# Kernel tuning notes

Hardware: AMD Instinct MI355X
Metric: run time of the kernel (lower is better)

## Reference

```python
import jax, jax.numpy as jnp
import numpy as np
from jax.scipy.special import erf, digamma, i0

B, L, D, H = 4, 4096, 512, 4
_MAX_SQRT_GRADIENT = 1000.0

@jax.custom_vjp
def sqrt_bound(x):
    return jnp.sqrt(x)

def _sb_fwd(x):
    return jnp.sqrt(x), x

def _sb_bwd(x, g):
    return (g / jnp.sqrt(jnp.clip(4.0 * x, 1.0 / _MAX_SQRT_GRADIENT**2, None)),)

sqrt_bound.defvjp(_sb_fwd, _sb_bwd)

def block_diag_linear(x, w):
    # x: [..., D], w: [h, bw, bw] block-diagonal weight
    h, bw, _ = w.shape
    xr = x.reshape(x.shape[:-1] + (h, bw))
    return jnp.einsum('...hi,hij->...hj', xr, w).reshape(x.shape)

def self_att_pool(x, num_heads):
    n_state = x.shape[-1] // num_heads
    attn = jax.nn.softmax(jnp.einsum('bld,bmd->blm', x, x) / np.float32(np.sqrt(n_state)), axis=-1)
    # max over the sequence axis of the attended values, keepdims -> [B,1,D]
    return jnp.max(jnp.einsum('blm,bmd->bld', attn, x), axis=-2, keepdims=True)

def ripple_transform_hybrid(t, mix_params):
    mix = jax.nn.softmax(mix_params)
    return mix[0] * digamma(t + 1.0) + mix[1] * i0(t)

def ripple_act(data, alpha, beta, mix_params, temperature=1.0):
    def f(d):
        norm = erf(d / (jnp.max(d) * alpha))
        return jnp.sum(ripple_transform_hybrid(norm * beta, mix_params))
    g = jnp.clip(jax.grad(f)(data), -1.0, 1.0)
    return jax.nn.softmax(-g / temperature, axis=-1)  # softmin

def ripplemoe_act(data, weights, alphas, beta, mix_params, temperature=1.0):
    def f(d):
        dmax = jnp.max(d)
        norm = erf(d[None] / (dmax * alphas[:, None, None]))  # [S,B,L]
        t = ripple_transform_hybrid(norm * beta, mix_params)
        w = jax.nn.softmax(weights)
        return jnp.sum(w[:, None, None] * t)
    g = jnp.clip(jax.grad(f)(data), -1.0, 1.0)
    return jax.nn.softmax(-g / temperature, axis=-1)  # softmin

def token_selection(x, cls_w, cls_b, token_weights, prelu_a, ts_weights, ts_alphas, ts_beta, ts_mix):
    scores = jnp.einsum('bld,sd->sbl', x, cls_w) + cls_b[:, None, None]  # [S,B,L]
    p = jnp.where(scores >= 0, scores, prelu_a * scores)  # PReLU
    ts = jax.nn.celu(p) * jax.nn.silu(p) + jax.nn.gelu(p, approximate=False)
    combined = jnp.einsum('s,sbl->bl', jax.nn.selu(token_weights[:, 0]), ts)
    _, idx = jax.lax.top_k(combined, combined.shape[-1])  # k = L, descending permutation
    vals = ts.sum(0)  # [B,L]
    b_idx = jnp.arange(combined.shape[0])[:, None]
    importance = jnp.ones_like(combined).at[b_idx, idx].add(vals)
    return (1.0 + ripplemoe_act(importance, ts_weights, ts_alphas, ts_beta, ts_mix))[..., None]

def _forward(x, attention_space, W_spatial, W_sil, W_ohead, W_out, w_ig, w_ag, a_param,
             cls_w, cls_b, token_weights, prelu_a, ts_weights, ts_alphas, ts_beta, ts_mix,
             pa1_alpha, pa1_beta, pa1_mix, pa2_alpha, pa2_beta, pa2_mix):
    spatial = jnp.einsum('bld,de->ble', x, attention_space) @ W_spatial.T
    # RG-LRU style gating
    gate_x = jax.nn.sigmoid(block_diag_linear(x, w_ig))
    gate_a = jax.nn.sigmoid(block_diag_linear(x, w_ag))
    log_a = -8.0 * jax.nn.softplus(a_param) * gate_a
    normalized_x = x * gate_x * sqrt_bound(1.0 - jnp.exp(2.0 * log_a))
    gated = jnp.exp(log_a) * self_att_pool(spatial, H) + normalized_x
    sparsity = ripple_act(gated @ W_sil.T, pa1_alpha, pa1_beta, pa1_mix)
    attn = (gated * sparsity) @ W_ohead.T
    sel = token_selection(x, cls_w, cls_b, token_weights, prelu_a, ts_weights, ts_alphas, ts_beta, ts_mix)
    out = ripple_act(attn * sel, pa2_alpha, pa2_beta, pa2_mix)
    return out @ W_out.T

def setup_inputs() -> dict:
    key = jax.random.key(0)
    ks = jax.random.split(key, 12)
    lim = float(1.0 / np.sqrt(D))
    xav = float(np.sqrt(6.0 / (2 * D)))
    bw = D // H
    u = jax.random.uniform(ks[8], (D,), jnp.float32, 0.9**2 + 1e-8, 0.999**2 + 1e-8)
    return {
        'x': jax.random.normal(ks[0], (B, L, D), jnp.float32),
        'attention_space': jax.random.uniform(ks[1], (D, D), jnp.float32, -xav, xav),
        'W_spatial': jax.random.uniform(ks[2], (D, D), jnp.float32, -lim, lim),
        'W_sil': jax.random.uniform(ks[3], (D, D), jnp.float32, -lim, lim),
        'W_ohead': jax.random.uniform(ks[4], (D, D), jnp.float32, -lim, lim),
        'W_out': jax.random.uniform(ks[5], (D, D), jnp.float32, -lim, lim),
        'w_ig': jax.random.normal(ks[6], (H, bw, bw), jnp.float32) * np.float32(np.sqrt(1.0 / bw)),
        'w_ag': jax.random.normal(ks[7], (H, bw, bw), jnp.float32) * np.float32(np.sqrt(1.0 / bw)),
        'a_param': jnp.log(jnp.exp(-0.5 * jnp.log(u)) - 1.0),
        'cls_w': jax.random.uniform(ks[9], (H, D), jnp.float32, -lim, lim),
        'cls_b': jax.random.uniform(ks[10], (H,), jnp.float32, -lim, lim),
        'token_weights': jax.random.normal(ks[11], (H, 1), jnp.float32),
        'prelu_a': jnp.array(0.25, jnp.float32),
        'ts_weights': jnp.ones(H, jnp.float32) / H,
        'ts_alphas': jnp.ones(H, jnp.float32),
        'ts_beta': jnp.array(1.0, jnp.float32),
        'ts_mix': jnp.full((2,), 0.5, jnp.float32),
        'pa1_alpha': jnp.array(1.0, jnp.float32),
        'pa1_beta': jnp.array(1.0, jnp.float32),
        'pa1_mix': jnp.full((2,), 0.5, jnp.float32),
        'pa2_alpha': jnp.array(1.0, jnp.float32),
        'pa2_beta': jnp.array(1.0, jnp.float32),
        'pa2_mix': jnp.full((2,), 0.5, jnp.float32),
    }

def reference(x, attention_space, W_spatial, W_sil, W_ohead, W_out, w_ig, w_ag, a_param,
              cls_w, cls_b, token_weights, prelu_a, ts_weights, ts_alphas, ts_beta, ts_mix,
              pa1_alpha, pa1_beta, pa1_mix, pa2_alpha, pa2_beta, pa2_mix):
    return _forward(x, attention_space, W_spatial, W_sil, W_ohead, W_out, w_ig, w_ag, a_param,
                    cls_w, cls_b, token_weights, prelu_a, ts_weights, ts_alphas, ts_beta, ts_mix,
                    pa1_alpha, pa1_beta, pa1_mix, pa2_alpha, pa2_beta, pa2_mix)
```

## Files before the change

### kernel.cpp

```cpp
#include <hip/hip_runtime.h>

typedef unsigned short ushort;
typedef unsigned int uint;
typedef unsigned long long u64;

#define DEV __device__ __forceinline__

typedef __attribute__((ext_vector_type(4))) float f32x4;
typedef __bf16 bf16x8 __attribute__((ext_vector_type(8)));
typedef __attribute__((ext_vector_type(4))) ushort u16x4;
typedef __attribute__((ext_vector_type(8))) ushort u16x8;

static constexpr int B_ = 4, L_ = 4096, D_ = 512;
static constexpr long NE = (long)B_ * L_ * D_;

DEV float b2f(ushort u) { return __uint_as_float(((uint)u) << 16); }
DEV ushort f2b(float f) {
    uint u = __float_as_uint(f);
    uint r = u + 0x7FFFu + ((u >> 16) & 1u);
    return (ushort)(r >> 16);
}
DEV uint mapF(float f) {
    uint b = __float_as_uint(f);
    return (b & 0x80000000u) ? ~b : (b | 0x80000000u);
}
DEV float unmapF(uint u) {
    uint b = (u & 0x80000000u) ? (u & 0x7FFFFFFFu) : ~u;
    return __uint_as_float(b);
}
DEV float rcp_(float x) { return __builtin_amdgcn_rcpf(x); }
DEV float fexp(float x) { return __builtin_amdgcn_exp2f(x * 1.44269504089f); }
DEV float sigm(float x) { return rcp_(1.f + fexp(-x)); }

DEV void gload16(const ushort* g, ushort* l) {
    __builtin_amdgcn_global_load_lds((const __attribute__((address_space(1))) void*)g,
                                     (__attribute__((address_space(3))) void*)l, 16, 0, 0);
}

DEV float trigamma1p(float t) {
    float x = t + 1.f;
    float acc = 0.f;
#pragma unroll
    for (int k = 0; k < 6; k++) { float xx = x + (float)k; acc += rcp_(xx * xx); }
    float y = x + 6.f;
    float iy = rcp_(y), iy2 = iy * iy;
    return acc + iy * (1.f + iy * (0.5f + iy * (0.166666667f + iy2 * (-0.0333333333f + iy2 * 0.0238095238f))));
}
DEV float besselI1(float t) {
    float q = 0.25f * t * t;
    return 0.5f * t * (1.f + q * (0.5f + q * (0.0833333333f + q * (0.00694444444f + q * (3.47222222e-4f + q * 1.15740741e-5f)))));
}
DEV float rippleH(float u, float beta, float mix0, float mix1) {
    float t = beta * erff(u);
    float Tp = mix0 * trigamma1p(t) + mix1 * besselI1(t);
    float ep = 1.12837917f * fexp(-u * u);
    return beta * Tp * ep;
}

DEV void gemm_core(const ushort* __restrict__ A, int lda,
                   const ushort* __restrict__ Bt, int ldb, int K,
                   ushort* __restrict__ Alds, ushort* __restrict__ Blds,
                   f32x4 (&acc)[4][4])
{
    const int tid = threadIdx.x;
    const int lane = tid & 63;
    const int wave = tid >> 6;
    const int wr = wave >> 1, wc = wave & 1;

    const int srow = wave * 16 + (lane >> 2);
    const int skc = (lane & 3) * 8;
    const ushort* Ag0 = A + (size_t)srow * lda + skc;
    const ushort* Ag1 = A + (size_t)(srow + 64) * lda + skc;
    const ushort* Bg0 = Bt + (size_t)srow * ldb + skc;
    const ushort* Bg1 = Bt + (size_t)(srow + 64) * ldb + skc;
    ushort* Al0 = Alds + wave * 512;
    ushort* Al1 = Alds + 2048 + wave * 512;
    ushort* Bl0 = Blds + wave * 512;
    ushort* Bl1 = Blds + 2048 + wave * 512;

    const int ar = wr * 64 + (lane & 15);
    const int br = wc * 64 + (lane & 15);
    const int kk = (lane >> 4) * 8;

    for (int k0 = 0; k0 < K; k0 += 32) {
        __syncthreads();
        gload16(Ag0 + k0, Al0);
        gload16(Ag1 + k0, Al1);
        gload16(Bg0 + k0, Bl0);
        gload16(Bg1 + k0, Bl1);
        __syncthreads();
        bf16x8 af[4], bfr[4];
#pragma unroll
        for (int mi = 0; mi < 4; mi++) af[mi] = *(const bf16x8*)&Alds[(ar + mi * 16) * 32 + kk];
#pragma unroll
        for (int ni = 0; ni < 4; ni++) bfr[ni] = *(const bf16x8*)&Blds[(br + ni * 16) * 32 + kk];
#pragma unroll
        for (int mi = 0; mi < 4; mi++)
#pragma unroll
            for (int ni = 0; ni < 4; ni++)
                acc[mi][ni] = __builtin_amdgcn_mfma_f32_16x16x32_bf16(af[mi], bfr[ni], acc[mi][ni], 0, 0, 0);
    }
}

template <int MODE, bool DOMAX>
__global__ __launch_bounds__(256, 2) void gemm_bt(
    const ushort* __restrict__ A, int lda,
    const ushort* __restrict__ Bt, int ldb,
    void* __restrict__ Cv, int ldc, int K,
    const float* __restrict__ rowScale, u64* __restrict__ pmax)
{
    __shared__ ushort Alds[128 * 32];
    __shared__ ushort Blds[128 * 32];
    const int row0 = blockIdx.y * 128, col0 = blockIdx.x * 128;
    f32x4 acc[4][4] = {};
    gemm_core(A + (size_t)row0 * lda, lda, Bt + (size_t)col0 * ldb, ldb, K, Alds, Blds, acc);

    const int tid = threadIdx.x;
    const int lane = tid & 63;
    const int wave = tid >> 6;
    const int wr = wave >> 1, wc = wave & 1;
    const int ocol = col0 + wc * 64 + (lane & 15);
    u64 lp = 0;
#pragma unroll
    for (int mi = 0; mi < 4; mi++) {
        const int rbase = row0 + wr * 64 + mi * 16 + (lane >> 4) * 4;
#pragma unroll
        for (int j = 0; j < 4; j++) {
            float sc = (MODE == 3) ? rowScale[rbase + j] : 1.f;
#pragma unroll
            for (int ni = 0; ni < 4; ni++) {
                float v = acc[mi][ni][j] * sc;
                int cc = ocol + ni * 16;
                if (MODE == 1) ((ushort*)Cv)[(size_t)(rbase + j) * ldc + cc] = f2b(v);
                else ((float*)Cv)[(size_t)(rbase + j) * ldc + cc] = v;
                if (DOMAX) {
                    uint idx = (uint)((rbase + j) * ldc + cc);
                    u64 p = ((u64)mapF(v) << 32) | (u64)(~idx);
                    lp = (p > lp) ? p : lp;
                }
            }
        }
    }
    if (DOMAX) {
#pragma unroll
        for (int off = 32; off > 0; off >>= 1) {
            u64 o = __shfl_xor(lp, off);
            lp = (o > lp) ? o : lp;
        }
        if (lane == 0) atomicMax(pmax, lp);
    }
}

__global__ __launch_bounds__(256, 2) void pv_split_k(const ushort* __restrict__ P, const ushort* __restrict__ Vt,
                                                     float* __restrict__ part)
{
    __shared__ ushort Alds[128 * 32];
    __shared__ ushort Blds[128 * 32];
    const int ks = blockIdx.z;
    const int row0 = blockIdx.y * 128, col0 = blockIdx.x * 128;
    f32x4 acc[4][4] = {};
    gemm_core(P + (size_t)row0 * 4096 + ks * 1024, 4096,
              Vt + (size_t)col0 * 4096 + ks * 1024, 4096, 1024, Alds, Blds, acc);

    float* C = part + (size_t)ks * 2097152 + (size_t)row0 * 512 + col0;
    const int tid = threadIdx.x;
    const int lane = tid & 63;
    const int wave = tid >> 6;
    const int wr = wave >> 1, wc = wave & 1;
    const int ocol = wc * 64 + (lane & 15);
#pragma unroll
    for (int mi = 0; mi < 4; mi++) {
        const int rl = wr * 64 + mi * 16 + (lane >> 4) * 4;
#pragma unroll
        for (int j = 0; j < 4; j++)
#pragma unroll
            for (int ni = 0; ni < 4; ni++)
                C[(size_t)(rl + j) * 512 + ocol + ni * 16] = acc[mi][ni][j];
    }
}

__global__ __launch_bounds__(256) void pool_combine_k(const float* __restrict__ part, uint* __restrict__ poolU)
{
    const int tid = threadIdx.x;
    const int l0 = blockIdx.x * 32;
    float m0 = -3.4e38f, m1 = -3.4e38f;
    for (int l = 0; l < 32; l++) {
        size_t off = (size_t)(l0 + l) * 512;
        float s0 = 0.f, s1 = 0.f;
#pragma unroll
        for (int ks = 0; ks < 4; ks++) {
            s0 += part[(size_t)ks * 2097152 + off + tid];
            s1 += part[(size_t)ks * 2097152 + off + tid + 256];
        }
        m0 = fmaxf(m0, s0); m1 = fmaxf(m1, s1);
    }
    atomicMax(&poolU[tid], mapF(m0));
    atomicMax(&poolU[tid + 256], mapF(m1));
}

__global__ __launch_bounds__(256, 2) void gate_gemm_k(const ushort* __restrict__ xb,
                                                      const ushort* __restrict__ wigT, const ushort* __restrict__ wagT,
                                                      ushort* __restrict__ gxab, ushort* __restrict__ gaab)
{
    __shared__ ushort Alds[128 * 32];
    __shared__ ushort Blds[128 * 32];
    const int which = blockIdx.x;
    const int h = blockIdx.z;
    const ushort* A = xb + (size_t)blockIdx.y * 128 * 512 + h * 128;
    const ushort* W = (which ? wagT : wigT) + (size_t)h * 16384;
    f32x4 acc[4][4] = {};
    gemm_core(A, 512, W, 128, 128, Alds, Blds, acc);

    ushort* C = (which ? gaab : gxab) + (size_t)blockIdx.y * 128 * 512 + h * 128;
    const int tid = threadIdx.x;
    const int lane = tid & 63;
    const int wave = tid >> 6;
    const int wr = wave >> 1, wc = wave & 1;
    const int ocol = wc * 64 + (lane & 15);
#pragma unroll
    for (int mi = 0; mi < 4; mi++) {
        const int rl = wr * 64 + mi * 16 + (lane >> 4) * 4;
#pragma unroll
        for (int j = 0; j < 4; j++)
#pragma unroll
            for (int ni = 0; ni < 4; ni++)
                C[(size_t)(rl + j) * 512 + ocol + ni * 16] = f2b(acc[mi][ni][j]);
    }
}

__global__ void convert_f2b_k(const float* __restrict__ s, ushort* __restrict__ d, long n4) {
    long i = (long)blockIdx.x * blockDim.x + threadIdx.x;
    long st = (long)gridDim.x * blockDim.x;
    for (; i < n4; i += st) {
        f32x4 v = ((const f32x4*)s)[i];
        u16x4 o;
        o[0] = f2b(v[0]); o[1] = f2b(v[1]); o[2] = f2b(v[2]); o[3] = f2b(v[3]);
        ((u16x4*)d)[i] = o;
    }
}

__global__ void convert_w4_k(const float* __restrict__ w0, const float* __restrict__ w1,
                             const float* __restrict__ w2, const float* __restrict__ w3,
                             ushort* __restrict__ dst) {
    const float* srcs[4] = {w0, w1, w2, w3};
    const float* s = srcs[blockIdx.y];
    ushort* d = dst + (size_t)blockIdx.y * 262144;
    int i = blockIdx.x * 256 + threadIdx.x;
    f32x4 v = ((const f32x4*)s)[i];
    u16x4 o;
    o[0] = f2b(v[0]); o[1] = f2b(v[1]); o[2] = f2b(v[2]); o[3] = f2b(v[3]);
    ((u16x4*)d)[i] = o;
}

template <bool SRCF32>
__global__ __launch_bounds__(256) void transpose_to_bf16(const void* __restrict__ srcv, ushort* __restrict__ dst, int R, int C) {
    __shared__ float tile[32][33];
    const int z = blockIdx.z;
    const float* sf = (const float*)srcv + (size_t)z * R * C;
    const ushort* sb = (const ushort*)srcv + (size_t)z * R * C;
    ushort* dz = dst + (size_t)z * R * C;
    const int tx = threadIdx.x & 31, ty = threadIdx.x >> 5;
    const int c = blockIdx.x * 32 + tx;
#pragma unroll
    for (int k = 0; k < 4; k++) {
        const int r = blockIdx.y * 32 + ty + k * 8;
        tile[ty + k * 8][tx] = SRCF32 ? sf[(size_t)r * C + c] : b2f(sb[(size_t)r * C + c]);
    }
    __syncthreads();
#pragma unroll
    for (int k = 0; k < 4; k++) {
        const int dr = blockIdx.x * 32 + ty + k * 8;
        const int dc = blockIdx.y * 32 + tx;
        dz[(size_t)dr * R + dc] = f2b(tile[tx][ty + k * 8]);
    }
}

__global__ __launch_bounds__(256) void transpose_gates_k(const float* __restrict__ wig, const float* __restrict__ wag,
                                                         ushort* __restrict__ wigT, ushort* __restrict__ wagT) {
    __shared__ float tile[32][33];
    const int which = blockIdx.z >> 2, h = blockIdx.z & 3;
    const float* src = (which ? wag : wig) + (size_t)h * 16384;
    ushort* dst = (which ? wagT : wigT) + (size_t)h * 16384;
    const int tx = threadIdx.x & 31, ty = threadIdx.x >> 5;
    const int c = blockIdx.x * 32 + tx;
#pragma unroll
    for (int k = 0; k < 4; k++) {
        const int r = blockIdx.y * 32 + ty + k * 8;
        tile[ty + k * 8][tx] = src[(size_t)r * 128 + c];
    }
    __syncthreads();
#pragma unroll
    for (int k = 0; k < 4; k++) {
        const int dr = blockIdx.x * 32 + ty + k * 8;
        const int dc = blockIdx.y * 32 + tx;
        dst[(size_t)dr * 128 + dc] = f2b(tile[tx][ty + k * 8]);
    }
}

__global__ void init_misc_k(uint* poolU, u64* pmax) {
    int i = blockIdx.x * 256 + threadIdx.x;
    if (i < 2048) poolU[i] = 0u;
    if (i < 4) pmax[i] = 0ull;
}
__global__ void sentinel_k(float* o) { o[threadIdx.x] = 1.0e6f; }

__global__ __launch_bounds__(256) void gates_gated_k(const float* __restrict__ x, const ushort* __restrict__ gxab,
                                                     const ushort* __restrict__ gaab, const float* __restrict__ a_param,
                                                     const uint* __restrict__ poolU, ushort* __restrict__ gatedb) {
    __shared__ float sp8[512];
    const int tid = threadIdx.x;
    for (int d = tid; d < 512; d += 256) {
        float a = a_param[d];
        sp8[d] = 8.f * (fmaxf(a, 0.f) + log1pf(expf(-fabsf(a))));
    }
    __syncthreads();
    long i = (long)blockIdx.x * blockDim.x + tid;
    long st = (long)gridDim.x * blockDim.x;
    const long n8 = NE >> 3;
    for (; i < n8; i += st) {
        u16x8 gx8 = ((const u16x8*)gxab)[i];
        u16x8 ga8 = ((const u16x8*)gaab)[i];
        f32x4 x0 = ((const f32x4*)x)[2 * i];
        f32x4 x1 = ((const f32x4*)x)[2 * i + 1];
        long e = i << 3;
        int b = (int)(e >> 21);
        int d0 = (int)(e & 511);
        u16x8 o;
#pragma unroll
        for (int j = 0; j < 8; j++) {
            float xv = (j < 4) ? x0[j] : x1[j - 4];
            float gx = sigm(b2f(gx8[j]));
            float ga = sigm(b2f(ga8[j]));
            float la = -sp8[d0 + j] * ga;
            float ea = fexp(la);
            float nx = xv * gx * sqrtf(fmaxf(1.f - fexp(2.f * la), 0.f));
            float pl = unmapF(poolU[b * 512 + d0 + j]);
            o[j] = f2b(ea * pl + nx);
        }
        ((u16x8*)gatedb)[i] = o;
    }
}

__global__ __launch_bounds__(256) void softmax_rows_k(const ushort* __restrict__ S, ushort* __restrict__ P, float scale) {
    __shared__ float red[256];
    const int tid = threadIdx.x;
    const ushort* row = S + (size_t)blockIdx.x * 4096;
    float vals[16];
    bf16x8 v0 = *(const bf16x8*)&row[tid * 16];
    bf16x8 v1 = *(const bf16x8*)&row[tid * 16 + 8];
    float mx = -3.4e38f;
#pragma unroll
    for (int k = 0; k < 8; k++) { vals[k] = (float)v0[k] * scale; mx = fmaxf(mx, vals[k]); }
#pragma unroll
    for (int k = 0; k < 8; k++) { vals[8 + k] = (float)v1[k] * scale; mx = fmaxf(mx, vals[8 + k]); }
    red[tid] = mx; __syncthreads();
    for (int s = 128; s > 0; s >>= 1) { if (tid < s) red[tid] = fmaxf(red[tid], red[tid + s]); __syncthreads(); }
    mx = red[0]; __syncthreads();
    float sum = 0.f;
#pragma unroll
    for (int k = 0; k < 16; k++) { vals[k] = fexp(vals[k] - mx); sum += vals[k]; }
    red[tid] = sum; __syncthreads();
    for (int s = 128; s > 0; s >>= 1) { if (tid < s) red[tid] += red[tid + s]; __syncthreads(); }
    float inv = rcp_(red[0]);
    ushort* prow = P + (size_t)blockIdx.x * 4096;
#pragma unroll
    for (int k = 0; k < 16; k++) prow[tid * 16 + k] = f2b(vals[k] * inv);
}

__global__ __launch_bounds__(256) void redmax1_k(const float* __restrict__ d, long n, float* __restrict__ bmax, int* __restrict__ bidx) {
    __shared__ float rv[256];
    __shared__ int ri[256];
    const int tid = threadIdx.x;
    long g = (long)blockIdx.x * 256 + tid;
    const long stride = (long)gridDim.x * 256;
    float bv = -3.4e38f; int bi = -1;
    for (long i = g; i < n; i += stride) {
        float v = d[i];
        if (v > bv) { bv = v; bi = (int)i; }
    }
    rv[tid] = bv; ri[tid] = bi; __syncthreads();
    for (int s = 128; s > 0; s >>= 1) {
        if (tid < s) {
            float ov = rv[tid + s]; int oi = ri[tid + s];
            if (oi >= 0 && (ri[tid] < 0 || ov > rv[tid] || (ov == rv[tid] && oi < ri[tid]))) { rv[tid] = ov; ri[tid] = oi; }
        }
        __syncthreads();
    }
    if (tid == 0) { bmax[blockIdx.x] = rv[0]; bidx[blockIdx.x] = ri[0]; }
}
__global__ __launch_bounds__(256) void redmax2_k(const float* __restrict__ bmax, const int* __restrict__ bidx, int n,
                                                 float* __restrict__ outM, int* __restrict__ outI) {
    __shared__ float rv[256];
    __shared__ int ri[256];
    const int tid = threadIdx.x;
    float bv = -3.4e38f; int bi = -1;
    for (int i = tid; i < n; i += 256) {
        float v = bmax[i]; int ix = bidx[i];
        if (ix >= 0 && (bi < 0 || v > bv || (v == bv && ix < bi))) { bv = v; bi = ix; }
    }
    rv[tid] = bv; ri[tid] = bi; __syncthreads();
    for (int s = 128; s > 0; s >>= 1) {
        if (tid < s) {
            float ov = rv[tid + s]; int oi = ri[tid + s];
            if (oi >= 0 && (ri[tid] < 0 || ov > rv[tid] || (ov == rv[tid] && oi < ri[tid]))) { rv[tid] = ov; ri[tid] = oi; }
        }
        __syncthreads();
    }
    if (tid == 0) { outM[0] = rv[0]; outI[0] = ri[0]; }
}

__global__ __launch_bounds__(256) void ripple_g_k(const float* __restrict__ d, float* __restrict__ gb, float* __restrict__ sspart,
                                                  const u64* __restrict__ pmax, const float* __restrict__ alpha_p,
                                                  const float* __restrict__ beta_p, const float* __restrict__ mix_p) {
    __shared__ float red[256];
    const int tid = threadIdx.x;
    const float M = unmapF((uint)(pmax[0] >> 32));
    const float alpha = alpha_p[0], beta = beta_p[0];
    float m0 = mix_p[0], m1 = mix_p[1];
    float mm = fmaxf(m0, m1);
    float e0 = fexp(m0 - mm), e1 = fexp(m1 - mm);
    float inv = rcp_(e0 + e1);
    float mix0 = e0 * inv, mix1 = e1 * inv;
    const float invMA = rcp_(M * alpha);
    float ss = 0.f;
    long g = (long)blockIdx.x * 256 + tid;
    const long stride = (long)gridDim.x * 256;
    for (long i = g; i < NE; i += stride) {
        float dv = d[i];
        float H = rippleH(dv * invMA, beta, mix0, mix1);
        gb[i] = H * invMA;
        ss += H * dv;
    }
    red[tid] = ss; __syncthreads();
    for (int s = 128; s > 0; s >>= 1) { if (tid < s) red[tid] += red[tid + s]; __syncthreads(); }
    if (tid == 0) sspart[blockIdx.x] = red[0];
}
__global__ __launch_bounds__(256) void redsum2_k(const float* __restrict__ part, int n, float* __restrict__ out) {
    __shared__ float red[256];
    const int tid = threadIdx.x;
    float s = 0.f;
    for (int i = tid; i < n; i += 256) s += part[i];
    red[tid] = s; __syncthreads();
    for (int q = 128; q > 0; q >>= 1) { if (tid < q) red[tid] += red[tid + q]; __syncthreads(); }
    if (tid == 0) out[0] = red[0];
}

template <int GS>
__global__ __launch_bounds__(256) void ripple_softmax_k(const float* __restrict__ gb,
                                                        const u64* __restrict__ pmax,
                                                        const float* __restrict__ ssTot, const float* __restrict__ alpha_p,
                                                        const ushort* __restrict__ gatedb, ushort* __restrict__ outb) {
    __shared__ float red[256];
    const int tid = threadIdx.x;
    const float M = unmapF((uint)(pmax[0] >> 32));
    const int amax = (int)(~(uint)(pmax[0] & 0xFFFFFFFFull));
    const float corr = ssTot[0] * rcp_(M * M * alpha_p[0]);
    long base = (long)blockIdx.x * 512;
    float g0 = gb[base + tid];
    float g1 = gb[base + tid + 256];
    if ((int)(base + tid) == amax) g0 -= corr;
    if ((int)(base + tid + 256) == amax) g1 -= corr;
    g0 = fminf(fmaxf(g0, -1.f), 1.f);
    g1 = fminf(fmaxf(g1, -1.f), 1.f);
    float mn = fminf(g0, g1);
    red[tid] = mn; __syncthreads();
    for (int s = 128; s > 0; s >>= 1) { if (tid < s) red[tid] = fminf(red[tid], red[tid + s]); __syncthreads(); }
    mn = red[0]; __syncthreads();
    float e0 = fexp(mn - g0), e1 = fexp(mn - g1);
    red[tid] = e0 + e1; __syncthreads();
    for (int s = 128; s > 0; s >>= 1) { if (tid < s) red[tid] += red[tid + s]; __syncthreads(); }
    float inv = rcp_(red[0]);
    if (GS) {
        outb[base + tid] = f2b(b2f(gatedb[base + tid]) * (e0 * inv));
        outb[base + tid + 256] = f2b(b2f(gatedb[base + tid + 256]) * (e1 * inv));
    } else {
        outb[base + tid] = f2b(e0 * inv);
        outb[base + tid + 256] = f2b(e1 * inv);
    }
}

__global__ __launch_bounds__(256) void ts1_k(const float* __restrict__ x, const float* __restrict__ cls_w,
                                             const float* __restrict__ cls_b, const float* __restrict__ tw,
                                             const float* __restrict__ prelu_a,
                                             float* __restrict__ combined, float* __restrict__ vals) {
    __shared__ float cw[2048];
    const int tid = threadIdx.x;
    for (int i = tid; i < 2048; i += 256) cw[i] = cls_w[i];
    __syncthreads();
    const int lane = tid & 63, wid = tid >> 6;
    const int row = blockIdx.x * 4 + wid;
    const float* xr = x + (size_t)row * 512 + lane * 8;
    float pa0 = 0, pa1 = 0, pa2 = 0, pa3 = 0;
#pragma unroll
    for (int j = 0; j < 8; j++) {
        float v = xr[j];
        int c = lane * 8 + j;
        pa0 += v * cw[c]; pa1 += v * cw[512 + c]; pa2 += v * cw[1024 + c]; pa3 += v * cw[1536 + c];
    }
#pragma unroll
    for (int o = 32; o > 0; o >>= 1) {
        pa0 += __shfl_down(pa0, o); pa1 += __shfl_down(pa1, o);
        pa2 += __shfl_down(pa2, o); pa3 += __shfl_down(pa3, o);
    }
    if (lane == 0) {
        float a = prelu_a[0];
        float sc[4] = {pa0, pa1, pa2, pa3};
        float comb = 0.f, vsum = 0.f;
#pragma unroll
        for (int s = 0; s < 4; s++) {
            float p = sc[s] + cls_b[s];
            p = (p >= 0.f) ? p : a * p;
            float cel = (p > 0.f) ? p : expm1f(p);
            float sil = p * sigm(p);
            float gel = 0.5f * p * (1.f + erff(p * 0.70710678f));
            float ts = cel * sil + gel;
            float ww = tw[s];
            float se = 1.05070099f * ((ww > 0.f) ? ww : 1.67326324f * expm1f(ww));
            comb += se * ts;
            vsum += ts;
        }
        combined[row] = comb;
        vals[row] = vsum;
    }
}

__global__ __launch_bounds__(256) void ts2a_k(const float* __restrict__ combined, int* __restrict__ rankp) {
    __shared__ float q[512];
    const int b = blockIdx.z;
    const int tid = threadIdx.x;
    const float* cr = combined + b * 4096;
    const int q0 = blockIdx.y * 512;
    for (int i = tid; i < 512; i += 256) q[i] = cr[q0 + i];
    __syncthreads();
    const int p = blockIdx.x * 256 + tid;
    const float cp = cr[p];
    const f32x4* q4 = (const f32x4*)q;
    int rank = 0;
#pragma unroll 8
    for (int i4 = 0; i4 < 128; i4++) {
        f32x4 v = q4[i4];
        int qb = q0 + i4 * 4;
        rank += (v[0] > cp) || (v[0] == cp && (qb + 0) < p);
        rank += (v[1] > cp) || (v[1] == cp && (qb + 1) < p);
        rank += (v[2] > cp) || (v[2] == cp && (qb + 2) < p);
        rank += (v[3] > cp) || (v[3] == cp && (qb + 3) < p);
    }
    rankp[((b * 8 + blockIdx.y) * 4096) + p] = rank;
}

__global__ __launch_bounds__(256) void ts2b_k(const int* __restrict__ rankp, const float* __restrict__ vals,
                                              float* __restrict__ imp) {
    const int b = blockIdx.y;
    const int p = blockIdx.x * 256 + threadIdx.x;
    int rank = 0;
#pragma unroll
    for (int c = 0; c < 8; c++) rank += rankp[((b * 8 + c) * 4096) + p];
    imp[b * 4096 + p] = 1.f + vals[b * 4096 + rank];
}

__global__ __launch_bounds__(256) void moe_g_k(const float* __restrict__ imp, float* __restrict__ gmoe,
                                               float* __restrict__ sspart, const float* __restrict__ scalM,
                                               const float* __restrict__ tsw, const float* __restrict__ tsa,
                                               const float* __restrict__ tsb, const float* __restrict__ tsmix) {
    __shared__ float red[256];
    const int tid = threadIdx.x;
    const float M = scalM[0];
    float w[4], invMA[4], invA[4];
    {
        float wm = fmaxf(fmaxf(tsw[0], tsw[1]), fmaxf(tsw[2], tsw[3]));
        float s = 0.f;
#pragma unroll
        for (int k = 0; k < 4; k++) { w[k] = fexp(tsw[k] - wm); s += w[k]; }
        float si = rcp_(s);
#pragma unroll
        for (int k = 0; k < 4; k++) { w[k] *= si; invMA[k] = rcp_(M * tsa[k]); invA[k] = rcp_(tsa[k]); }
    }
    const float beta = tsb[0];
    float m0 = tsmix[0], m1 = tsmix[1];
    float mm = fmaxf(m0, m1);
    float e0 = fexp(m0 - mm), e1 = fexp(m1 - mm);
    float minv = rcp_(e0 + e1);
    const float mix0 = e0 * minv, mix1 = e1 * minv;

    float ss = 0.f;
    int i = blockIdx.x * 256 + tid;
    const int stride = gridDim.x * 256;
    for (; i < 65536; i += stride) {
        float dv = imp[i];
        float gbv = 0.f;
#pragma unroll
        for (int s = 0; s < 4; s++) {
            float H = rippleH(dv * invMA[s], beta, mix0, mix1);
            gbv += w[s] * H * invMA[s];
            ss += w[s] * H * dv * invA[s];
        }
        gmoe[i] = gbv;
    }
    red[tid] = ss; __syncthreads();
    for (int s = 128; s > 0; s >>= 1) { if (tid < s) red[tid] += red[tid + s]; __syncthreads(); }
    if (tid == 0) sspart[blockIdx.x] = red[0];
}

__global__ __launch_bounds__(256) void moe_sel_k(const float* __restrict__ gmoe, const float* __restrict__ scalM,
                                                 const int* __restrict__ scalI, const float* __restrict__ ssTot,
                                                 float* __restrict__ sel) {
    __shared__ float red[256];
    const int tid = threadIdx.x;
    const int b = blockIdx.x;
    const float M = scalM[0];
    const int amax = scalI[0];
    const float corr = ssTot[0] * rcp_(M * M);
    float g[16];
    float mn = 3.4e38f;
#pragma unroll
    for (int k = 0; k < 16; k++) {
        int i = b * 4096 + tid + k * 256;
        float v = gmoe[i];
        if (i == amax) v -= corr;
        v = fminf(fmaxf(v, -1.f), 1.f);
        g[k] = v;
        mn = fminf(mn, v);
    }
    red[tid] = mn; __syncthreads();
    for (int s = 128; s > 0; s >>= 1) { if (tid < s) red[tid] = fminf(red[tid], red[tid + s]); __syncthreads(); }
    mn = red[0]; __syncthreads();
    float sum = 0.f;
#pragma unroll
    for (int k = 0; k < 16; k++) { g[k] = fexp(mn - g[k]); sum += g[k]; }
    red[tid] = sum; __syncthreads();
    for (int s = 128; s > 0; s >>= 1) { if (tid < s) red[tid] += red[tid + s]; __syncthreads(); }
    float inv = rcp_(red[0]);
#pragma unroll
    for (int k = 0; k < 16; k++) sel[b * 4096 + tid + k * 256] = 1.f + g[k] * inv;
}

static constexpr size_t OFF_XB    = 0;
static constexpr size_t OFF_TMPB  = 16777216;
static constexpr size_t OFF_SPB   = 33554432;
static constexpr size_t OFF_SPT   = 50331648;
static constexpr size_t OFF_DBUF  = 67108864;
static constexpr size_t OFF_HBUF  = 100663296;
static constexpr size_t OFF_GATB  = 134217728;
static constexpr size_t OFF_NXB   = 150994944;
static constexpr size_t OFF_EAB   = 167772160;
static constexpr size_t OFF_AST   = 184549376;
static constexpr size_t OFF_WSP   = 185073664;
static constexpr size_t OFF_WSIL  = 185597952;
static constexpr size_t OFF_WOH   = 186122240;
static constexpr size_t OFF_WOUT  = 186646528;
static constexpr size_t OFF_WIGT  = 187170816;
static constexpr size_t OFF_WAGT  = 187301888;
static constexpr size_t OFF_POOL  = 187432960;
static constexpr size_t OFF_SCAL  = 187441152;
static constexpr size_t OFF_SCALI = 187441408;
static constexpr size_t OFF_BMAX  = 187441664;
static constexpr size_t OFF_BIDX  = 187449856;
static constexpr size_t OFF_SSP   = 187458048;
static constexpr size_t OFF_COMB  = 187466240;
static constexpr size_t OFF_VALS  = 187728384;
static constexpr size_t OFF_IMP   = 187990528;
static constexpr size_t OFF_GMOE  = 188252672;
static constexpr size_t OFF_SEL   = 188514816;
static constexpr size_t WS_NEED   = 188776960;

extern "C" void kernel_launch(void* const* d_in, const int* in_sizes, int n_in,
                              void* d_out, int out_size, void* d_ws, size_t ws_size,
                              hipStream_t stream)
{
    (void)in_sizes; (void)n_in; (void)out_size;
    const float* x    = (const float*)d_in[0];
    const float* AS   = (const float*)d_in[1];
    const float* Wsp  = (const float*)d_in[2];
    const float* Wsil = (const float*)d_in[3];
    const float* Woh  = (const float*)d_in[4];
    const float* Wout = (const float*)d_in[5];
    const float* wig  = (const float*)d_in[6];
    const float* wag  = (const float*)d_in[7];
    const float* a_param = (const float*)d_in[8];
    const float* cls_w = (const float*)d_in[9];
    const float* cls_b = (const float*)d_in[10];
    const float* tokw  = (const float*)d_in[11];
    const float* prelu = (const float*)d_in[12];
    const float* tsw   = (const float*)d_in[13];
    const float* tsa   = (const float*)d_in[14];
    const float* tsb   = (const float*)d_in[15];
    const float* tsmix = (const float*)d_in[16];
    const float* p1a = (const float*)d_in[17];
    const float* p1b = (const float*)d_in[18];
    const float* p1m = (const float*)d_in[19];
    const float* p2a = (const float*)d_in[20];
    const float* p2b = (const float*)d_in[21];
    const float* p2m = (const float*)d_in[22];
    float* out = (float*)d_out;

    char* w = (char*)d_ws;
    if (ws_size < WS_NEED) { sentinel_k<<<1, 256, 0, stream>>>(out); return; }

    ushort* xb    = (ushort*)(w + OFF_XB);
    ushort* tmpb  = (ushort*)(w + OFF_TMPB);
    ushort* spb   = (ushort*)(w + OFF_SPB);
    ushort* spT   = (ushort*)(w + OFF_SPT);
    float*  dbuf  = (float*)(w + OFF_DBUF);
    float*  Hbuf  = (float*)(w + OFF_HBUF);
    ushort* Sb    = (ushort*)(w + OFF_DBUF);
    ushort* Pb    = (ushort*)(w + OFF_HBUF);
    float*  pvpart= (float*)(w + OFF_XB);
    int*    rankp = (int*)(w + OFF_DBUF);
    ushort* gatedb= (ushort*)(w + OFF_GATB);
    ushort* gxab  = (ushort*)(w + OFF_NXB);
    ushort* gaab  = (ushort*)(w + OFF_EAB);
    ushort* ASt   = (ushort*)(w + OFF_AST);
    ushort* Wspb  = (ushort*)(w + OFF_WSP);
    ushort* Wsilb = (ushort*)(w + OFF_WSIL);
    ushort* Wohb  = (ushort*)(w + OFF_WOH);
    ushort* Woutb = (ushort*)(w + OFF_WOUT);
    ushort* wigT  = (ushort*)(w + OFF_WIGT);
    ushort* wagT  = (ushort*)(w + OFF_WAGT);
    uint*   poolU = (uint*)(w + OFF_POOL);
    float*  scal  = (float*)(w + OFF_SCAL);
    u64*    pmax  = (u64*)(w + OFF_SCAL + 128);
    int*    scalI = (int*)(w + OFF_SCALI);
    float*  bmax  = (float*)(w + OFF_BMAX);
    int*    bidx  = (int*)(w + OFF_BIDX);
    float*  sspart= (float*)(w + OFF_SSP);
    float*  comb  = (float*)(w + OFF_COMB);
    float*  vals  = (float*)(w + OFF_VALS);
    float*  imp   = (float*)(w + OFF_IMP);
    float*  gmoe  = (float*)(w + OFF_GMOE);
    float*  sel   = (float*)(w + OFF_SEL);
    ushort* gsb     = tmpb;
    ushort* probs2b = xb;

    convert_f2b_k<<<2048, 256, 0, stream>>>(x, xb, NE >> 2);
    convert_w4_k<<<dim3(256, 4), 256, 0, stream>>>(Wsp, Wsil, Woh, Wout, Wspb);
    transpose_to_bf16<true><<<dim3(16, 16, 1), 256, 0, stream>>>(AS, ASt, 512, 512);
    transpose_gates_k<<<dim3(4, 4, 8), 256, 0, stream>>>(wig, wag, wigT, wagT);
    init_misc_k<<<8, 256, 0, stream>>>(poolU, pmax);

    gate_gemm_k<<<dim3(2, 128, 4), 256, 0, stream>>>(xb, wigT, wagT, gxab, gaab);

    gemm_bt<1, false><<<dim3(4, 128), 256, 0, stream>>>(xb, 512, ASt, 512, tmpb, 512, 512, nullptr, nullptr);
    gemm_bt<1, false><<<dim3(4, 128), 256, 0, stream>>>(tmpb, 512, Wspb, 512, spb, 512, 512, nullptr, nullptr);

    transpose_to_bf16<false><<<dim3(16, 128, 4), 256, 0, stream>>>(spb, spT, 4096, 512);
    const float sc128 = 0.0883883476f;
    for (int b = 0; b < 4; b++) {
        const ushort* spB = spb + (size_t)b * L_ * D_;
        gemm_bt<1, false><<<dim3(32, 32), 256, 0, stream>>>(spB, 512, spB, 512, Sb, 4096, 512, nullptr, nullptr);
        softmax_rows_k<<<4096, 256, 0, stream>>>(Sb, Pb, sc128);
        pv_split_k<<<dim3(4, 32, 4), 256, 0, stream>>>(Pb, spT + (size_t)b * D_ * L_, pvpart);
        pool_combine_k<<<128, 256, 0, stream>>>(pvpart, poolU + b * 512);
    }

    gates_gated_k<<<1024, 256, 0, stream>>>(x, gxab, gaab, a_param, poolU, gatedb);

    gemm_bt<0, true><<<dim3(4, 128), 256, 0, stream>>>(gatedb, 512, Wsilb, 512, dbuf, 512, 512, nullptr, &pmax[0]);
    ripple_g_k<<<2048, 256, 0, stream>>>(dbuf, Hbuf, sspart, &pmax[0], p1a, p1b, p1m);
    redsum2_k<<<1, 256, 0, stream>>>(sspart, 2048, &scal[1]);
    ripple_softmax_k<1><<<16384, 256, 0, stream>>>(Hbuf, &pmax[0], &scal[1], p1a, gatedb, gsb);

    ts1_k<<<4096, 256, 0, stream>>>(x, cls_w, cls_b, tokw, prelu, comb, vals);
    ts2a_k<<<dim3(16, 8, 4), 256, 0, stream>>>(comb, rankp);
    ts2b_k<<<dim3(16, 4), 256, 0, stream>>>(rankp, vals, imp);
    redmax1_k<<<64, 256, 0, stream>>>(imp, 65536, bmax, bidx);
    redmax2_k<<<1, 256, 0, stream>>>(bmax, bidx, 64, &scal[4], &scalI[2]);
    moe_g_k<<<64, 256, 0, stream>>>(imp, gmoe, sspart, &scal[4], tsw, tsa, tsb, tsmix);
    redsum2_k<<<1, 256, 0, stream>>>(sspart, 64, &scal[5]);
    moe_sel_k<<<4, 256, 0, stream>>>(gmoe, &scal[4], &scalI[2], &scal[5], sel);

    gemm_bt<3, true><<<dim3(4, 128), 256, 0, stream>>>(gsb, 512, Wohb, 512, dbuf, 512, 512, sel, &pmax[1]);

    ripple_g_k<<<2048, 256, 0, stream>>>(dbuf, Hbuf, sspart, &pmax[1], p2a, p2b, p2m);
    redsum2_k<<<1, 256, 0, stream>>>(sspart, 2048, &scal[3]);
    ripple_softmax_k<0><<<16384, 256, 0, stream>>>(Hbuf, &pmax[1], &scal[3], p2a, nullptr, probs2b);

    gemm_bt<0, false><<<dim3(4, 128), 256, 0, stream>>>(probs2b, 512, Woutb, 512, out, 512, 512, nullptr, nullptr);
}
```

Baseline: 641.6 us.

## Double-buffer GEMM LDS tiles and add XCD-aware workgroup swizzle

The shared GEMM core now uses two LDS buffers, so the global-to-LDS load of the next K slice is issued before the MFMAs on the current slice, with one barrier per iteration instead of two. This is meant to hide global load latency behind matrix math. Separately, gemm_bt and pv_split_k remap block indices so that consecutive tiles land on the same XCD, aiming for better L2 reuse. The cost is doubled LDS per block, which may limit occupancy. There is also a possible race, since the prefetch writes into the other buffer while slower waves could still be reading it.

```diff
diff --git a/kernel.cpp b/kernel.cpp
--- a/kernel.cpp
+++ b/kernel.cpp
@@ -35,6 +35,13 @@
 DEV void gload16(const ushort* g, ushort* l) {
     __builtin_amdgcn_global_load_lds((const __attribute__((address_space(1))) void*)g,
                                      (__attribute__((address_space(3))) void*)l, 16, 0, 0);
+}
+
+DEV int xcd_swz(int b, int nwg) {
+    int q = nwg >> 3, r = nwg & 7;
+    int x = b & 7, i = b >> 3;
+    int base = (x < r) ? x * (q + 1) : r * (q + 1) + (x - r) * q;
+    return base + i;
 }
 
 DEV float trigamma1p(float t) {
@@ -73,32 +80,39 @@
     const ushort* Ag1 = A + (size_t)(srow + 64) * lda + skc;
     const ushort* Bg0 = Bt + (size_t)srow * ldb + skc;
     const ushort* Bg1 = Bt + (size_t)(srow + 64) * ldb + skc;
-    ushort* Al0 = Alds + wave * 512;
-    ushort* Al1 = Alds + 2048 + wave * 512;
-    ushort* Bl0 = Blds + wave * 512;
-    ushort* Bl1 = Blds + 2048 + wave * 512;
+    const int wb = wave * 512;
 
     const int ar = wr * 64 + (lane & 15);
     const int br = wc * 64 + (lane & 15);
     const int kk = (lane >> 4) * 8;
 
+    gload16(Ag0, Alds + wb);
+    gload16(Ag1, Alds + 2048 + wb);
+    gload16(Bg0, Blds + wb);
+    gload16(Bg1, Blds + 2048 + wb);
+    __syncthreads();
+
+    int cur = 0;
     for (int k0 = 0; k0 < K; k0 += 32) {
-        __syncthreads();
-        gload16(Ag0 + k0, Al0);
-        gload16(Ag1 + k0, Al1);
-        gload16(Bg0 + k0, Bl0);
-        gload16(Bg1 + k0, Bl1);
-        __syncthreads();
+        const int nb = cur ^ 1;
+        if (k0 + 32 < K) {
+            gload16(Ag0 + k0 + 32, Alds + nb * 4096 + wb);
+            gload16(Ag1 + k0 + 32, Alds + nb * 4096 + 2048 + wb);
+            gload16(Bg0 + k0 + 32, Blds + nb * 4096 + wb);
+            gload16(Bg1 + k0 + 32, Blds + nb * 4096 + 2048 + wb);
+        }
         bf16x8 af[4], bfr[4];
 #pragma unroll
-        for (int mi = 0; mi < 4; mi++) af[mi] = *(const bf16x8*)&Alds[(ar + mi * 16) * 32 + kk];
-#pragma unroll
-        for (int ni = 0; ni < 4; ni++) bfr[ni] = *(const bf16x8*)&Blds[(br + ni * 16) * 32 + kk];
+        for (int mi = 0; mi < 4; mi++) af[mi] = *(const bf16x8*)&Alds[cur * 4096 + (ar + mi * 16) * 32 + kk];
+#pragma unroll
+        for (int ni = 0; ni < 4; ni++) bfr[ni] = *(const bf16x8*)&Blds[cur * 4096 + (br + ni * 16) * 32 + kk];
 #pragma unroll
         for (int mi = 0; mi < 4; mi++)
 #pragma unroll
             for (int ni = 0; ni < 4; ni++)
                 acc[mi][ni] = __builtin_amdgcn_mfma_f32_16x16x32_bf16(af[mi], bfr[ni], acc[mi][ni], 0, 0, 0);
+        __syncthreads();
+        cur = nb;
     }
 }
 
@@ -109,9 +123,12 @@
     void* __restrict__ Cv, int ldc, int K,
     const float* __restrict__ rowScale, u64* __restrict__ pmax)
 {
-    __shared__ ushort Alds[128 * 32];
-    __shared__ ushort Blds[128 * 32];
-    const int row0 = blockIdx.y * 128, col0 = blockIdx.x * 128;
+    __shared__ ushort Alds[2 * 128 * 32];
+    __shared__ ushort Blds[2 * 128 * 32];
+    const int nwg = gridDim.x * gridDim.y;
+    const int s = xcd_swz(blockIdx.y * gridDim.x + blockIdx.x, nwg);
+    const int bx = s % gridDim.x, by = s / gridDim.x;
+    const int row0 = by * 128, col0 = bx * 128;
     f32x4 acc[4][4] = {};
     gemm_core(A + (size_t)row0 * lda, lda, Bt + (size_t)col0 * ldb, ldb, K, Alds, Blds, acc);
 
@@ -154,10 +171,13 @@
 __global__ __launch_bounds__(256, 2) void pv_split_k(const ushort* __restrict__ P, const ushort* __restrict__ Vt,
                                                      float* __restrict__ part)
 {
-    __shared__ ushort Alds[128 * 32];
-    __shared__ ushort Blds[128 * 32];
+    __shared__ ushort Alds[2 * 128 * 32];
+    __shared__ ushort Blds[2 * 128 * 32];
     const int ks = blockIdx.z;
-    const int row0 = blockIdx.y * 128, col0 = blockIdx.x * 128;
+    const int nwg = gridDim.x * gridDim.y;
+    const int s = xcd_swz(blockIdx.y * gridDim.x + blockIdx.x, nwg);
+    const int bx = s % gridDim.x, by = s / gridDim.x;
+    const int row0 = by * 128, col0 = bx * 128;
     f32x4 acc[4][4] = {};
     gemm_core(P + (size_t)row0 * 4096 + ks * 1024, 4096,
               Vt + (size_t)col0 * 4096 + ks * 1024, 4096, 1024, Alds, Blds, acc);
@@ -202,8 +222,8 @@
                                                       const ushort* __restrict__ wigT, const ushort* __restrict__ wagT,
                                                       ushort* __restrict__ gxab, ushort* __restrict__ gaab)
 {
-    __shared__ ushort Alds[128 * 32];
-    __shared__ ushort Blds[128 * 32];
+    __shared__ ushort Alds[2 * 128 * 32];
+    __shared__ ushort Blds[2 * 128 * 32];
     const int which = blockIdx.x;
     const int h = blockIdx.z;
     const ushort* A = xb + (size_t)blockIdx.y * 128 * 512 + h * 128;
```

Result: no change. 648.1 us (+1.0%).
